# Kernel tuning notes

Measured on AMD Instinct MI355X. Metric: run time of the kernel, lower is better.

## Reference

```python
import jax, jax.numpy as jnp
import numpy as np

VOCAB = 9
D = 128      # EMBED_DIM
S = 64       # SEQ_LEN / context_length
B = 512      # batch
NH = 4       # num_heads
DH = D // NH # head dim = 32
NB = 2       # num_blocks
EPS = 1e-5


def setup_inputs() -> dict:
    key = jax.random.key(0)
    ks = jax.random.split(key, 10)
    rn = lambda k, shape: jax.random.normal(k, shape, jnp.float32) * 0.02
    return {
        "x": jax.random.randint(ks[0], (B, S), 0, VOCAB),
        "emb": rn(ks[1], (VOCAB, D)),
        "ln1_w": jnp.ones((NB, D), jnp.float32),          # pre-sLSTM LayerNorm weight
        "Wg": rn(ks[2], (NB, 4, NH, DH, DH)),             # headwise gate projections (i,f,z,o)
        "R": rn(ks[3], (NB, NH, DH, 4 * DH)),             # recurrent kernels per head
        "bias": rn(ks[4], (NB, NH, 4, DH)),               # cell bias per head/gate
        "gn_w": jnp.ones((NB, D), jnp.float32),           # multi-head (group) norm weight
        "ln2_w": jnp.ones((NB, D), jnp.float32),          # pre-FF LayerNorm weight
        "ff_up_w": rn(ks[5], (NB, 2 * D, D)),             # gated FF up projection
        "ff_down_w": rn(ks[6], (NB, D, D)),               # FF down projection
        "post_w": jnp.ones((D,), jnp.float32),            # post-blocks LayerNorm weight
        "proj_w": rn(ks[7], (VOCAB, D)),
        "proj_b": jnp.zeros((VOCAB,), jnp.float32),
    }


def _layernorm(x, w):
    mu = x.mean(-1, keepdims=True)
    var = x.var(-1, keepdims=True)
    return (x - mu) * jax.lax.rsqrt(var + EPS) * w


def _mh_groupnorm(h, w):
    # h: [B,S,NH,DH] -> normalize over DH per head, scale by per-channel w [D]
    mu = h.mean(-1, keepdims=True)
    var = h.var(-1, keepdims=True)
    hn = (h - mu) * jax.lax.rsqrt(var + EPS)
    return hn.reshape(h.shape[0], h.shape[1], D) * w


def _slstm_layer(xh, Wg, R, b):
    # xh: [B,S,NH,DH]; Wg: [4,NH,DH,DH]; R: [NH,DH,4*DH]; b: [NH,4,DH]
    gx = jnp.einsum('bsnh,gnkh->sbngk', xh, Wg)  # [S,B,NH,4,DH] gate preacts (i,f,z,o)

    def step(carry, g):
        h, c, n, m = carry  # each [B,NH,DH]
        ry = jnp.einsum('bnh,nhk->bnk', h, R).reshape(h.shape[0], NH, 4, DH)
        raw = g + ry + b
        i_r, f_r, z_r, o_r = raw[:, :, 0], raw[:, :, 1], raw[:, :, 2], raw[:, :, 3]
        logfplusm = m + jax.nn.log_sigmoid(f_r)
        mnew = jnp.maximum(i_r, logfplusm)            # stabilizer
        ig = jnp.exp(i_r - mnew)
        fg = jnp.exp(logfplusm - mnew)
        cnew = fg * c + ig * jnp.tanh(z_r)
        nnew = fg * n + ig
        hnew = jax.nn.sigmoid(o_r) * cnew / nnew
        return (hnew, cnew, nnew, mnew), hnew

    z0 = jnp.zeros((xh.shape[0], NH, DH), xh.dtype)
    _, hs = jax.lax.scan(step, (z0, z0, z0, z0), gx)
    return hs.transpose(1, 0, 2, 3)  # [B,S,NH,DH]


def reference(x, emb, ln1_w, Wg, R, bias, gn_w, ln2_w, ff_up_w, ff_down_w, post_w, proj_w, proj_b):
    h = emb[x]  # [B,S,D]
    for bi in range(NB):
        xn = _layernorm(h, ln1_w[bi])
        y = _slstm_layer(xn.reshape(h.shape[0], S, NH, DH), Wg[bi], R[bi], bias[bi])
        h = h + _mh_groupnorm(y, gn_w[bi])
        xn = _layernorm(h, ln2_w[bi])
        up = xn @ ff_up_w[bi].T                       # [B,S,2D]
        gate, upv = up[..., :D], up[..., D:]
        h = h + (jax.nn.gelu(gate, approximate=False) * upv) @ ff_down_w[bi].T
    h = _layernorm(h, post_w)
    return h @ proj_w.T + proj_b  # [B,S,VOCAB]
```

## Files before the change

kernel.cpp:

```cpp
#include <hip/hip_runtime.h>
#include <math.h>

#define D      128
#define S_LEN  64
#define B_SZ   512
#define NH     4
#define DH     32
#define NB     2
#define VOCAB  9
#define EPS    1e-5f
#define NTOK   (B_SZ * S_LEN)

template <int CTRL>
__device__ __forceinline__ float dppf(float x) {
    return __int_as_float(__builtin_amdgcn_update_dpp(
        0, __float_as_int(x), CTRL, 0xF, 0xF, true));
}
__device__ __forceinline__ float wsum64(float x) {
    x += dppf<0x111>(x);
    x += dppf<0x112>(x);
    x += dppf<0x114>(x);
    x += dppf<0x118>(x);
    x += dppf<0x142>(x);
    x += dppf<0x143>(x);
    return __int_as_float(__builtin_amdgcn_readlane(__float_as_int(x), 63));
}

__device__ __forceinline__ int xc3(int t, int c) { return c ^ (((t >> 1) & 7) << 2); }
__device__ __forceinline__ int xa (int t, int c) { return c ^ ((t & 7) << 2); }

__device__ __forceinline__ float dot4(float4 a, float4 b, float c) {
    c = fmaf(a.x, b.x, c);
    c = fmaf(a.y, b.y, c);
    c = fmaf(a.z, b.z, c);
    c = fmaf(a.w, b.w, c);
    return c;
}

__global__ __launch_bounds__(256) void k_embed(const int* __restrict__ x,
                                               const float* __restrict__ emb,
                                               float* __restrict__ h,
                                               float* __restrict__ stats)
{
    int lane = threadIdx.x & 63;
    int wv   = threadIdx.x >> 6;
    int tok  = blockIdx.x * 4 + wv;
    int xi   = x[tok];
    float2 v = ((const float2*)(emb + xi * D))[lane];
    ((float2*)(h + (size_t)tok * D))[lane] = v;
    float s1 = wsum64(v.x + v.y);
    float s2 = wsum64(v.x * v.x + v.y * v.y);
    float mu  = s1 * (1.0f / D);
    float var = s2 * (1.0f / D) - mu * mu;
    if (lane == 0) {
        stats[tok * 2]     = mu;
        stats[tok * 2 + 1] = rsqrtf(var + EPS);
    }
}

__global__ __launch_bounds__(64, 2) void k_gxscan(
    const float* __restrict__ Wg,
    const float* __restrict__ Rm,
    const float* __restrict__ bias,
    const float* __restrict__ lnw,
    const float* __restrict__ gnw,
    const float* __restrict__ stats,
    float* __restrict__ h)
{
    __shared__ float xl[64 * 32];

    int b    = blockIdx.x >> 2;
    int n    = blockIdx.x & 3;
    int lane = threadIdx.x;
    int e    = lane >> 1;
    int sub  = lane & 1;
    int colA = sub * DH + e;

    size_t tok0 = (size_t)b * S_LEN;

    {
        const float* hrow = h + (tok0 + lane) * D + n * DH;
        float2 st = ((const float2*)stats)[tok0 + lane];
        float mu = st.x, rs = st.y;
        #pragma unroll
        for (int q = 0; q < 8; ++q) {
            float4 v = *(const float4*)(hrow + q * 4);
            float4 o;
            o.x = (v.x - mu) * rs * lnw[n * DH + q * 4 + 0];
            o.y = (v.y - mu) * rs * lnw[n * DH + q * 4 + 1];
            o.z = (v.z - mu) * rs * lnw[n * DH + q * 4 + 2];
            o.w = (v.w - mu) * rs * lnw[n * DH + q * 4 + 3];
            *(float4*)&xl[lane * 32 + ((q ^ (lane & 7)) << 2)] = o;
        }
    }
    __syncthreads();

    int gA = sub;
    int gB = 2 + sub;
    const float* wrowA = Wg + ((size_t)(gA * NH + n) * DH + e) * DH;
    const float* wrowB = Wg + ((size_t)(gB * NH + n) * DH + e) * DH;
    float4 wgA[8], wgB[8], wrA[8], wrB[8];
    #pragma unroll
    for (int cc = 0; cc < 8; ++cc) {
        wgA[cc] = *(const float4*)(wrowA + cc * 4);
        wgB[cc] = *(const float4*)(wrowB + cc * 4);
        #pragma unroll
        for (int j = 0; j < 4; ++j) {
            ((float*)&wrA[cc])[j] = Rm[(n * DH + cc * 4 + j) * 128 + colA];
            ((float*)&wrB[cc])[j] = Rm[(n * DH + cc * 4 + j) * 128 + 64 + colA];
        }
    }
    float biasA = bias[(n * 4 + gA) * DH + e];
    float biasB = bias[(n * 4 + gB) * DH + e];
    float gw    = gnw[n * DH + e];

    auto gxpair = [&](int s, float& ga, float& gb) {
        float a0 = 0.f, a1 = 0.f, b0 = 0.f, b1 = 0.f;
        #pragma unroll
        for (int cc = 0; cc < 8; cc += 2) {
            float4 x0 = *(const float4*)&xl[s * 32 + ((cc ^ (s & 7)) << 2)];
            float4 x1 = *(const float4*)&xl[s * 32 + (((cc + 1) ^ (s & 7)) << 2)];
            a0 = dot4(x0, wgA[cc],     a0);
            a1 = dot4(x1, wgA[cc + 1], a1);
            b0 = dot4(x0, wgB[cc],     b0);
            b1 = dot4(x1, wgB[cc + 1], b1);
        }
        ga = biasA + (a0 + a1);
        gb = biasB + (b0 + b1);
    };

    float curA[8], curB[8], nxtA[8], nxtB[8];
    #pragma unroll
    for (int i = 0; i < 8; ++i) gxpair(i, curA[i], curB[i]);

    float hu[32];
    #pragma unroll
    for (int i = 0; i < 32; ++i) hu[i] = 0.f;
    float c = 0.f, nacc = 0.f, m = 0.f;

    float* hb = h + tok0 * D + n * DH;
    float pHR[4];
    #pragma unroll
    for (int k = 0; k < 4; ++k) pHR[k] = hb[k * D + e];

    for (int ch = 0; ch < 8; ++ch) {
        #pragma unroll
        for (int i = 0; i < 8; ++i) {
            int s = ch * 8 + i;
            if (ch < 7) gxpair(s + 8, nxtA[i], nxtB[i]);
            int sp = (s + 4 < S_LEN) ? s + 4 : S_LEN - 1;
            float nHR = hb[sp * D + e];

            float r0=0,r1=0,r2=0,r3=0,q0=0,q1=0,q2=0,q3=0;
            #pragma unroll
            for (int cc = 0; cc < 8; ++cc) {
                r0 = fmaf(hu[cc*4+0], wrA[cc].x, r0);
                r1 = fmaf(hu[cc*4+1], wrA[cc].y, r1);
                r2 = fmaf(hu[cc*4+2], wrA[cc].z, r2);
                r3 = fmaf(hu[cc*4+3], wrA[cc].w, r3);
                q0 = fmaf(hu[cc*4+0], wrB[cc].x, q0);
                q1 = fmaf(hu[cc*4+1], wrB[cc].y, q1);
                q2 = fmaf(hu[cc*4+2], wrB[cc].z, q2);
                q3 = fmaf(hu[cc*4+3], wrB[cc].w, q3);
            }
            float rawA = curA[i] + ((r0 + r1) + (r2 + r3));
            float rawB = curB[i] + ((q0 + q1) + (q2 + q3));

            float xA = dppf<0xB1>(rawA);
            float xB = dppf<0xB1>(rawB);
            float i_r = sub ? xA   : rawA;
            float f_r = sub ? rawA : xA;
            float z_r = sub ? xB   : rawB;
            float o_r = sub ? rawB : xB;

            float lsf  = fminf(f_r, 0.f)
                       - 0.69314718055994531f * __log2f(1.0f + __expf(-fabsf(f_r)));
            float lfm  = m + lsf;
            float mnew = fmaxf(i_r, lfm);
            float ig   = __expf(i_r - mnew);
            float fg   = __expf(lfm - mnew);
            float t    = __expf(2.f * z_r);
            float tz   = 1.f - 2.f / (t + 1.f);
            c    = fg * c + ig * tz;
            nacc = fg * nacc + ig;
            m    = mnew;
            float hv = c / (nacc * (1.f + __expf(-o_r)));

            float s1 = wsum64(hv);
            float s2 = wsum64(hv * hv);
            float mu2 = s1 * (1.f / 64.f);
            float var = s2 * (1.f / 64.f) - mu2 * mu2;
            float hn  = (hv - mu2) * rsqrtf(var + EPS) * gw;

            if (!sub) hb[s * D + e] = pHR[0] + hn;

            #pragma unroll
            for (int i2 = 0; i2 < 32; ++i2)
                hu[i2] = __int_as_float(
                    __builtin_amdgcn_readlane(__float_as_int(hv), 2 * i2));

            pHR[0]=pHR[1]; pHR[1]=pHR[2]; pHR[2]=pHR[3]; pHR[3]=nHR;
        }
        #pragma unroll
        for (int i = 0; i < 8; ++i) { curA[i] = nxtA[i]; curB[i] = nxtB[i]; }
    }
}

template <int LAST>
__global__ __launch_bounds__(256, 2) void k_ff(float* __restrict__ h,
                                               const float* __restrict__ ln2w,
                                               const float* __restrict__ wup,
                                               const float* __restrict__ wdn,
                                               float* __restrict__ stats_out,
                                               const float* __restrict__ lastw,
                                               const float* __restrict__ projw,
                                               const float* __restrict__ projb,
                                               float* __restrict__ out)
{
    __shared__ float xs[32 * 128];
    __shared__ float as_[32 * 64];
    __shared__ float wt[2 * 32 * 64];

    int tid  = threadIdx.x;
    int lane = tid & 63;
    int wv   = tid >> 6;
    size_t tok0 = (size_t)blockIdx.x * 32;

    for (int i = 0; i < 8; ++i) {
        int t = wv * 8 + i;
        const float* hp = h + (tok0 + t) * D;
        float v1 = hp[lane], v2 = hp[64 + lane];
        float s1 = wsum64(v1 + v2);
        float s2 = wsum64(v1 * v1 + v2 * v2);
        float mu = s1 * (1.0f / D);
        float rs = rsqrtf(s2 * (1.0f / D) - mu * mu + EPS);
        xs[t * D + xc3(t, lane)]      = (v1 - mu) * rs * ln2w[lane];
        xs[t * D + xc3(t, lane + 64)] = (v2 - mu) * rs * ln2w[64 + lane];
    }

    int q     = tid & 7;
    int r0    = tid >> 3;
    int goff0 = r0 * D + q * 4;
    int goff1 = (r0 + 32) * D + q * 4;
    int s0    = r0 ^ (q << 2);
    int kb    = q * 4;

    auto ffld = [&](int id, float4* pre) {
        int p = (id >= 6) ? 1 : 0;
        int j = id - p * 6;
        const float* b0;
        const float* b1;
        if (j < 4) { b0 = wup + (p * 64) * D + j * 32;
                     b1 = wup + (128 + p * 64) * D + j * 32; }
        else       { int jj = j - 4;
                     b0 = wdn + p * 64 + jj * 32;
                     b1 = wdn + 64 * D + p * 64 + jj * 32; }
        pre[0] = *(const float4*)(b0 + goff0);
        pre[1] = *(const float4*)(b0 + goff1);
        pre[2] = *(const float4*)(b1 + goff0);
        pre[3] = *(const float4*)(b1 + goff1);
    };
    auto fst = [&](const float4* pre) {
        #pragma unroll
        for (int cc = 0; cc < 4; ++cc) {
            const float* p0 = (const float*)&pre[0];
            const float* p1 = (const float*)&pre[1];
            const float* p2 = (const float*)&pre[2];
            const float* p3 = (const float*)&pre[3];
            wt[(kb + cc) * 64 + s0]           = p0[cc];
            wt[(kb + cc) * 64 + s0 + 32]      = p1[cc];
            wt[2048 + (kb + cc) * 64 + s0]      = p2[cc];
            wt[2048 + (kb + cc) * 64 + s0 + 32] = p3[cc];
        }
    };

    int ti = tid >> 4;
    int oi = tid & 15;
    int t0 = ti * 2;
    int o0 = oi * 4;

    float accd[2][2][4];
    #pragma unroll
    for (int a1 = 0; a1 < 2; ++a1)
        #pragma unroll
        for (int j = 0; j < 2; ++j)
            #pragma unroll
            for (int cc = 0; cc < 4; ++cc) accd[a1][j][cc] = 0.f;

    float4 pre[4];
    ffld(0, pre);
    int id = 1;

    #pragma unroll
    for (int p = 0; p < 2; ++p) {
        float accg[2][4], accv[2][4];
        #pragma unroll
        for (int j = 0; j < 2; ++j)
            #pragma unroll
            for (int cc = 0; cc < 4; ++cc) { accg[j][cc] = 0.f; accv[j][cc] = 0.f; }

        for (int c4 = 0; c4 < 4; ++c4) {
            __syncthreads();
            fst(pre);
            if (id < 12) ffld(id, pre);
            ++id;
            __syncthreads();
            int kc = c4 * 32;
            #pragma unroll
            for (int k4 = 0; k4 < 8; ++k4) {
                float4 a0 = *(const float4*)&xs[t0 * D + xc3(t0, kc + k4 * 4)];
                float4 a1v = *(const float4*)&xs[(t0 + 1) * D + xc3(t0 + 1, kc + k4 * 4)];
                int ws = k4 << 2;
                #pragma unroll
                for (int i = 0; i < 4; ++i) {
                    int k = k4 * 4 + i;
                    float4 bg = *(const float4*)&wt[k * 64 + (o0 ^ ws)];
                    float4 bv = *(const float4*)&wt[2048 + k * 64 + (o0 ^ ws)];
                    float ax0 = ((const float*)&a0)[i];
                    float ax1 = ((const float*)&a1v)[i];
                    accg[0][0] = fmaf(ax0, bg.x, accg[0][0]);
                    accg[0][1] = fmaf(ax0, bg.y, accg[0][1]);
                    accg[0][2] = fmaf(ax0, bg.z, accg[0][2]);
                    accg[0][3] = fmaf(ax0, bg.w, accg[0][3]);
                    accg[1][0] = fmaf(ax1, bg.x, accg[1][0]);
                    accg[1][1] = fmaf(ax1, bg.y, accg[1][1]);
                    accg[1][2] = fmaf(ax1, bg.z, accg[1][2]);
                    accg[1][3] = fmaf(ax1, bg.w, accg[1][3]);
                    accv[0][0] = fmaf(ax0, bv.x, accv[0][0]);
                    accv[0][1] = fmaf(ax0, bv.y, accv[0][1]);
                    accv[0][2] = fmaf(ax0, bv.z, accv[0][2]);
                    accv[0][3] = fmaf(ax0, bv.w, accv[0][3]);
                    accv[1][0] = fmaf(ax1, bv.x, accv[1][0]);
                    accv[1][1] = fmaf(ax1, bv.y, accv[1][1]);
                    accv[1][2] = fmaf(ax1, bv.z, accv[1][2]);
                    accv[1][3] = fmaf(ax1, bv.w, accv[1][3]);
                }
            }
        }
        #pragma unroll
        for (int j = 0; j < 2; ++j) {
            int t = t0 + j;
            float4 av;
            float* ap = (float*)&av;
            #pragma unroll
            for (int cc = 0; cc < 4; ++cc) {
                float g = accg[j][cc];
                float u = accv[j][cc];
                ap[cc] = 0.5f * g * (1.0f + erff(g * 0.70710678118654752f)) * u;
            }
            *(float4*)&as_[t * 64 + xa(t, o0)] = av;
        }
        for (int c2 = 0; c2 < 2; ++c2) {
            __syncthreads();
            fst(pre);
            if (id < 12) ffld(id, pre);
            ++id;
            __syncthreads();
            int kc = c2 * 32;
            #pragma unroll
            for (int k4 = 0; k4 < 8; ++k4) {
                float4 a0 = *(const float4*)&as_[t0 * 64 + xa(t0, kc + k4 * 4)];
                float4 a1v = *(const float4*)&as_[(t0 + 1) * 64 + xa(t0 + 1, kc + k4 * 4)];
                int ws = k4 << 2;
                #pragma unroll
                for (int i = 0; i < 4; ++i) {
                    int k = k4 * 4 + i;
                    float4 b0v = *(const float4*)&wt[k * 64 + (o0 ^ ws)];
                    float4 b1v = *(const float4*)&wt[2048 + k * 64 + (o0 ^ ws)];
                    float ax0 = ((const float*)&a0)[i];
                    float ax1 = ((const float*)&a1v)[i];
                    accd[0][0][0] = fmaf(ax0, b0v.x, accd[0][0][0]);
                    accd[0][0][1] = fmaf(ax0, b0v.y, accd[0][0][1]);
                    accd[0][0][2] = fmaf(ax0, b0v.z, accd[0][0][2]);
                    accd[0][0][3] = fmaf(ax0, b0v.w, accd[0][0][3]);
                    accd[0][1][0] = fmaf(ax1, b0v.x, accd[0][1][0]);
                    accd[0][1][1] = fmaf(ax1, b0v.y, accd[0][1][1]);
                    accd[0][1][2] = fmaf(ax1, b0v.z, accd[0][1][2]);
                    accd[0][1][3] = fmaf(ax1, b0v.w, accd[0][1][3]);
                    accd[1][0][0] = fmaf(ax0, b1v.x, accd[1][0][0]);
                    accd[1][0][1] = fmaf(ax0, b1v.y, accd[1][0][1]);
                    accd[1][0][2] = fmaf(ax0, b1v.z, accd[1][0][2]);
                    accd[1][0][3] = fmaf(ax0, b1v.w, accd[1][0][3]);
                    accd[1][1][0] = fmaf(ax1, b1v.x, accd[1][1][0]);
                    accd[1][1][1] = fmaf(ax1, b1v.y, accd[1][1][1]);
                    accd[1][1][2] = fmaf(ax1, b1v.z, accd[1][1][2]);
                    accd[1][1][3] = fmaf(ax1, b1v.w, accd[1][1][3]);
                }
            }
        }
    }

    #pragma unroll
    for (int j = 0; j < 2; ++j) {
        int t = t0 + j;
        size_t tok = tok0 + t;
        #pragma unroll
        for (int a1 = 0; a1 < 2; ++a1) {
            int cb = a1 * 64 + o0;
            float4 hres = *(const float4*)(h + tok * D + cb);
            float4 hn;
            hn.x = hres.x + accd[a1][j][0];
            hn.y = hres.y + accd[a1][j][1];
            hn.z = hres.z + accd[a1][j][2];
            hn.w = hres.w + accd[a1][j][3];
            if (!LAST) *(float4*)(h + tok * D + cb) = hn;
            *(float4*)&xs[t * D + xc3(t, cb)] = hn;
        }
    }
    __syncthreads();

    if (!LAST) {
        for (int i = 0; i < 8; ++i) {
            int t = wv * 8 + i;
            float v1 = xs[t * D + xc3(t, lane)];
            float v2 = xs[t * D + xc3(t, lane + 64)];
            float s1 = wsum64(v1 + v2);
            float s2 = wsum64(v1 * v1 + v2 * v2);
            float mu = s1 * (1.0f / D);
            float rs = rsqrtf(s2 * (1.0f / D) - mu * mu + EPS);
            if (lane == 0) {
                stats_out[(tok0 + t) * 2]     = mu;
                stats_out[(tok0 + t) * 2 + 1] = rs;
            }
        }
    } else {
        float pw1[VOCAB], pw2[VOCAB], pb[VOCAB];
        #pragma unroll
        for (int v = 0; v < VOCAB; ++v) {
            pw1[v] = projw[v * D + lane];
            pw2[v] = projw[v * D + 64 + lane];
            pb[v]  = projb[v];
        }
        for (int i = 0; i < 8; ++i) {
            int t = wv * 8 + i;
            float v1 = xs[t * D + xc3(t, lane)];
            float v2 = xs[t * D + xc3(t, lane + 64)];
            float s1 = wsum64(v1 + v2);
            float s2 = wsum64(v1 * v1 + v2 * v2);
            float mu = s1 * (1.0f / D);
            float rs = rsqrtf(s2 * (1.0f / D) - mu * mu + EPS);
            float x1 = (v1 - mu) * rs * lastw[lane];
            float x2 = (v2 - mu) * rs * lastw[64 + lane];
            #pragma unroll
            for (int v = 0; v < VOCAB; ++v) {
                float pp = wsum64(fmaf(x1, pw1[v], x2 * pw2[v]));
                if (lane == 0) out[(tok0 + t) * VOCAB + v] = pp + pb[v];
            }
        }
    }
}

extern "C" void kernel_launch(void* const* d_in, const int* in_sizes, int n_in,
                              void* d_out, int out_size, void* d_ws, size_t ws_size,
                              hipStream_t stream)
{
    const int*   x     = (const int*)  d_in[0];
    const float* emb   = (const float*)d_in[1];
    const float* ln1   = (const float*)d_in[2];
    const float* Wg    = (const float*)d_in[3];
    const float* Rm    = (const float*)d_in[4];
    const float* bias  = (const float*)d_in[5];
    const float* gnw   = (const float*)d_in[6];
    const float* ln2   = (const float*)d_in[7];
    const float* wup   = (const float*)d_in[8];
    const float* wdn   = (const float*)d_in[9];
    const float* postw = (const float*)d_in[10];
    const float* projw = (const float*)d_in[11];
    const float* projb = (const float*)d_in[12];
    float* out   = (float*)d_out;
    float* hbuf  = (float*)d_ws;
    float* stats = hbuf + (size_t)NTOK * D;

    k_embed<<<NTOK / 4, 256, 0, stream>>>(x, emb, hbuf, stats);

    for (int bi = 0; bi < NB; ++bi) {
        k_gxscan<<<B_SZ * NH, 64, 0, stream>>>(Wg + bi * 4 * NH * DH * DH,
                                               Rm + bi * NH * DH * 4 * DH,
                                               bias + bi * NH * 4 * DH,
                                               ln1 + bi * D,
                                               gnw + bi * D,
                                               stats, hbuf);
        if (bi == 0)
            k_ff<0><<<NTOK / 32, 256, 0, stream>>>(hbuf, ln2 + bi * D,
                                                   wup + bi * 2 * D * D,
                                                   wdn + bi * D * D,
                                                   stats, nullptr, nullptr,
                                                   nullptr, nullptr);
        else
            k_ff<1><<<NTOK / 32, 256, 0, stream>>>(hbuf, ln2 + bi * D,
                                                   wup + bi * 2 * D * D,
                                                   wdn + bi * D * D,
                                                   nullptr, postw, projw,
                                                   projb, out);
    }
}
```

Baseline: 354.7 us.

## Split gate-projection and recurrence into producer/consumer waves with shared-memory double buffer

The sLSTM scan kernel now runs two waves per block. One wave computes the input gate projections for the next chunk of 8 timesteps into a double-buffered shared array, while the other runs the serial recurrence on the current chunk. This takes the gate-projection FMAs and their weight registers off the latency-critical recurrent wave and should let it run at higher occupancy. The cost is a block barrier per chunk and a producer wave that sits idle for much of each chunk.

```diff
diff --git a/kernel.cpp b/kernel.cpp
--- a/kernel.cpp
+++ b/kernel.cpp
@@ -58,7 +58,7 @@
     }
 }
 
-__global__ __launch_bounds__(64, 2) void k_gxscan(
+__global__ __launch_bounds__(128, 4) void k_gxscan(
     const float* __restrict__ Wg,
     const float* __restrict__ Rm,
     const float* __restrict__ bias,
@@ -67,142 +67,170 @@
     const float* __restrict__ stats,
     float* __restrict__ h)
 {
-    __shared__ float xl[64 * 32];
+    __shared__ float xl[64][32];
+    __shared__ float gxb[2][8][128];
 
     int b    = blockIdx.x >> 2;
     int n    = blockIdx.x & 3;
-    int lane = threadIdx.x;
+    int tid  = threadIdx.x;
+    int wv   = tid >> 6;
+    int lane = tid & 63;
+    size_t tok0 = (size_t)b * S_LEN;
+
+    {
+        int t  = tid >> 1;
+        int hf = tid & 1;
+        const float* hrow = h + (tok0 + t) * D + n * DH + hf * 16;
+        float2 st = ((const float2*)stats)[tok0 + t];
+        float mu = st.x, rs = st.y;
+        #pragma unroll
+        for (int q = 0; q < 4; ++q) {
+            int qq = hf * 4 + q;
+            float4 v = *(const float4*)(hrow + q * 4);
+            float4 o;
+            o.x = (v.x - mu) * rs * lnw[n * DH + qq * 4 + 0];
+            o.y = (v.y - mu) * rs * lnw[n * DH + qq * 4 + 1];
+            o.z = (v.z - mu) * rs * lnw[n * DH + qq * 4 + 2];
+            o.w = (v.w - mu) * rs * lnw[n * DH + qq * 4 + 3];
+            *(float4*)&xl[t][(qq ^ (t & 7)) << 2] = o;
+        }
+    }
+
     int e    = lane >> 1;
     int sub  = lane & 1;
     int colA = sub * DH + e;
 
-    size_t tok0 = (size_t)b * S_LEN;
-
-    {
-        const float* hrow = h + (tok0 + lane) * D + n * DH;
-        float2 st = ((const float2*)stats)[tok0 + lane];
-        float mu = st.x, rs = st.y;
-        #pragma unroll
-        for (int q = 0; q < 8; ++q) {
-            float4 v = *(const float4*)(hrow + q * 4);
-            float4 o;
-            o.x = (v.x - mu) * rs * lnw[n * DH + q * 4 + 0];
-            o.y = (v.y - mu) * rs * lnw[n * DH + q * 4 + 1];
-            o.z = (v.z - mu) * rs * lnw[n * DH + q * 4 + 2];
-            o.w = (v.w - mu) * rs * lnw[n * DH + q * 4 + 3];
-            *(float4*)&xl[lane * 32 + ((q ^ (lane & 7)) << 2)] = o;
-        }
-    }
-    __syncthreads();
-
-    int gA = sub;
-    int gB = 2 + sub;
-    const float* wrowA = Wg + ((size_t)(gA * NH + n) * DH + e) * DH;
-    const float* wrowB = Wg + ((size_t)(gB * NH + n) * DH + e) * DH;
-    float4 wgA[8], wgB[8], wrA[8], wrB[8];
-    #pragma unroll
-    for (int cc = 0; cc < 8; ++cc) {
-        wgA[cc] = *(const float4*)(wrowA + cc * 4);
-        wgB[cc] = *(const float4*)(wrowB + cc * 4);
-        #pragma unroll
-        for (int j = 0; j < 4; ++j) {
-            ((float*)&wrA[cc])[j] = Rm[(n * DH + cc * 4 + j) * 128 + colA];
-            ((float*)&wrB[cc])[j] = Rm[(n * DH + cc * 4 + j) * 128 + 64 + colA];
-        }
-    }
-    float biasA = bias[(n * 4 + gA) * DH + e];
-    float biasB = bias[(n * 4 + gB) * DH + e];
-    float gw    = gnw[n * DH + e];
-
-    auto gxpair = [&](int s, float& ga, float& gb) {
-        float a0 = 0.f, a1 = 0.f, b0 = 0.f, b1 = 0.f;
-        #pragma unroll
-        for (int cc = 0; cc < 8; cc += 2) {
-            float4 x0 = *(const float4*)&xl[s * 32 + ((cc ^ (s & 7)) << 2)];
-            float4 x1 = *(const float4*)&xl[s * 32 + (((cc + 1) ^ (s & 7)) << 2)];
-            a0 = dot4(x0, wgA[cc],     a0);
-            a1 = dot4(x1, wgA[cc + 1], a1);
-            b0 = dot4(x0, wgB[cc],     b0);
-            b1 = dot4(x1, wgB[cc + 1], b1);
-        }
-        ga = biasA + (a0 + a1);
-        gb = biasB + (b0 + b1);
+    float4 wrA[8], wrB[8];
+    float4 wg1[8], wg2[8];
+    float  gw = 0.f, bs1 = 0.f, bs2 = 0.f;
+
+    if (wv == 0) {
+        #pragma unroll
+        for (int cc = 0; cc < 8; ++cc)
+            #pragma unroll
+            for (int j = 0; j < 4; ++j) {
+                ((float*)&wrA[cc])[j] = Rm[(n * DH + cc * 4 + j) * 128 + colA];
+                ((float*)&wrB[cc])[j] = Rm[(n * DH + cc * 4 + j) * 128 + 64 + colA];
+            }
+        gw = gnw[n * DH + e];
+    } else {
+        int g1 = lane >> 5, e1 = lane & 31;
+        int g2 = g1 + 2;
+        const float* r1 = Wg + ((size_t)(g1 * NH + n) * DH + e1) * DH;
+        const float* r2 = Wg + ((size_t)(g2 * NH + n) * DH + e1) * DH;
+        #pragma unroll
+        for (int cc = 0; cc < 8; ++cc) {
+            wg1[cc] = *(const float4*)(r1 + cc * 4);
+            wg2[cc] = *(const float4*)(r2 + cc * 4);
+        }
+        bs1 = bias[(n * 4 + g1) * DH + e1];
+        bs2 = bias[(n * 4 + g2) * DH + e1];
+    }
+
+    auto compute_chunk = [&](int ch) {
+        int bufi = ch & 1;
+        #pragma unroll
+        for (int i = 0; i < 8; ++i) {
+            int t = ch * 8 + i;
+            float a0 = 0.f, a1 = 0.f, b0 = 0.f, b1 = 0.f;
+            #pragma unroll
+            for (int cc = 0; cc < 8; cc += 2) {
+                float4 x0 = *(const float4*)&xl[t][(cc ^ (t & 7)) << 2];
+                float4 x1 = *(const float4*)&xl[t][((cc + 1) ^ (t & 7)) << 2];
+                a0 = dot4(x0, wg1[cc],     a0);
+                a1 = dot4(x1, wg1[cc + 1], a1);
+                b0 = dot4(x0, wg2[cc],     b0);
+                b1 = dot4(x1, wg2[cc + 1], b1);
+            }
+            gxb[bufi][i][lane]      = bs1 + (a0 + a1);
+            gxb[bufi][i][64 + lane] = bs2 + (b0 + b1);
+        }
     };
-
-    float curA[8], curB[8], nxtA[8], nxtB[8];
-    #pragma unroll
-    for (int i = 0; i < 8; ++i) gxpair(i, curA[i], curB[i]);
 
     float hu[32];
     #pragma unroll
     for (int i = 0; i < 32; ++i) hu[i] = 0.f;
     float c = 0.f, nacc = 0.f, m = 0.f;
-
     float* hb = h + tok0 * D + n * DH;
     float pHR[4];
-    #pragma unroll
-    for (int k = 0; k < 4; ++k) pHR[k] = hb[k * D + e];
+    if (wv == 0) {
+        #pragma unroll
+        for (int k = 0; k < 4; ++k) pHR[k] = hb[k * D + e];
+    }
+
+    __syncthreads();
+    if (wv == 1) compute_chunk(0);
+    __syncthreads();
 
     for (int ch = 0; ch < 8; ++ch) {
-        #pragma unroll
-        for (int i = 0; i < 8; ++i) {
-            int s = ch * 8 + i;
-            if (ch < 7) gxpair(s + 8, nxtA[i], nxtB[i]);
-            int sp = (s + 4 < S_LEN) ? s + 4 : S_LEN - 1;
-            float nHR = hb[sp * D + e];
-
-            float r0=0,r1=0,r2=0,r3=0,q0=0,q1=0,q2=0,q3=0;
-            #pragma unroll
-            for (int cc = 0; cc < 8; ++cc) {
-                r0 = fmaf(hu[cc*4+0], wrA[cc].x, r0);
-                r1 = fmaf(hu[cc*4+1], wrA[cc].y, r1);
-                r2 = fmaf(hu[cc*4+2], wrA[cc].z, r2);
-                r3 = fmaf(hu[cc*4+3], wrA[cc].w, r3);
-                q0 = fmaf(hu[cc*4+0], wrB[cc].x, q0);
-                q1 = fmaf(hu[cc*4+1], wrB[cc].y, q1);
-                q2 = fmaf(hu[cc*4+2], wrB[cc].z, q2);
-                q3 = fmaf(hu[cc*4+3], wrB[cc].w, q3);
-            }
-            float rawA = curA[i] + ((r0 + r1) + (r2 + r3));
-            float rawB = curB[i] + ((q0 + q1) + (q2 + q3));
-
-            float xA = dppf<0xB1>(rawA);
-            float xB = dppf<0xB1>(rawB);
-            float i_r = sub ? xA   : rawA;
-            float f_r = sub ? rawA : xA;
-            float z_r = sub ? xB   : rawB;
-            float o_r = sub ? rawB : xB;
-
-            float lsf  = fminf(f_r, 0.f)
-                       - 0.69314718055994531f * __log2f(1.0f + __expf(-fabsf(f_r)));
-            float lfm  = m + lsf;
-            float mnew = fmaxf(i_r, lfm);
-            float ig   = __expf(i_r - mnew);
-            float fg   = __expf(lfm - mnew);
-            float t    = __expf(2.f * z_r);
-            float tz   = 1.f - 2.f / (t + 1.f);
-            c    = fg * c + ig * tz;
-            nacc = fg * nacc + ig;
-            m    = mnew;
-            float hv = c / (nacc * (1.f + __expf(-o_r)));
-
-            float s1 = wsum64(hv);
-            float s2 = wsum64(hv * hv);
-            float mu2 = s1 * (1.f / 64.f);
-            float var = s2 * (1.f / 64.f) - mu2 * mu2;
-            float hn  = (hv - mu2) * rsqrtf(var + EPS) * gw;
-
-            if (!sub) hb[s * D + e] = pHR[0] + hn;
-
-            #pragma unroll
-            for (int i2 = 0; i2 < 32; ++i2)
-                hu[i2] = __int_as_float(
-                    __builtin_amdgcn_readlane(__float_as_int(hv), 2 * i2));
-
-            pHR[0]=pHR[1]; pHR[1]=pHR[2]; pHR[2]=pHR[3]; pHR[3]=nHR;
-        }
-        #pragma unroll
-        for (int i = 0; i < 8; ++i) { curA[i] = nxtA[i]; curB[i] = nxtB[i]; }
+        if (wv == 1) {
+            if (ch < 7) compute_chunk(ch + 1);
+        } else {
+            int bufi = ch & 1;
+            float gA_[8], gB_[8];
+            #pragma unroll
+            for (int i = 0; i < 8; ++i) {
+                gA_[i] = gxb[bufi][i][colA];
+                gB_[i] = gxb[bufi][i][64 + colA];
+            }
+            #pragma unroll
+            for (int i = 0; i < 8; ++i) {
+                int s = ch * 8 + i;
+                int sp = (s + 4 < S_LEN) ? s + 4 : S_LEN - 1;
+                float nHR = hb[sp * D + e];
+
+                float r0=0,r1=0,r2=0,r3=0,q0=0,q1=0,q2=0,q3=0;
+                #pragma unroll
+                for (int cc = 0; cc < 8; ++cc) {
+                    r0 = fmaf(hu[cc*4+0], wrA[cc].x, r0);
+                    r1 = fmaf(hu[cc*4+1], wrA[cc].y, r1);
+                    r2 = fmaf(hu[cc*4+2], wrA[cc].z, r2);
+                    r3 = fmaf(hu[cc*4+3], wrA[cc].w, r3);
+                    q0 = fmaf(hu[cc*4+0], wrB[cc].x, q0);
+                    q1 = fmaf(hu[cc*4+1], wrB[cc].y, q1);
+                    q2 = fmaf(hu[cc*4+2], wrB[cc].z, q2);
+                    q3 = fmaf(hu[cc*4+3], wrB[cc].w, q3);
+                }
+                float rawA = gA_[i] + ((r0 + r1) + (r2 + r3));
+                float rawB = gB_[i] + ((q0 + q1) + (q2 + q3));
+
+                float xA = dppf<0xB1>(rawA);
+                float xB = dppf<0xB1>(rawB);
+                float i_r = sub ? xA   : rawA;
+                float f_r = sub ? rawA : xA;
+                float z_r = sub ? xB   : rawB;
+                float o_r = sub ? rawB : xB;
+
+                float lsf  = fminf(f_r, 0.f)
+                           - 0.69314718055994531f * __log2f(1.0f + __expf(-fabsf(f_r)));
+                float lfm  = m + lsf;
+                float mnew = fmaxf(i_r, lfm);
+                float ig   = __expf(i_r - mnew);
+                float fg   = __expf(lfm - mnew);
+                float t    = __expf(2.f * z_r);
+                float tz   = 1.f - 2.f / (t + 1.f);
+                c    = fg * c + ig * tz;
+                nacc = fg * nacc + ig;
+                m    = mnew;
+                float hv = c / (nacc * (1.f + __expf(-o_r)));
+
+                float s1 = wsum64(hv);
+                float s2 = wsum64(hv * hv);
+                float mu2 = s1 * (1.f / 64.f);
+                float var = s2 * (1.f / 64.f) - mu2 * mu2;
+                float hn  = (hv - mu2) * rsqrtf(var + EPS) * gw;
+
+                if (!sub) hb[s * D + e] = pHR[0] + hn;
+
+                #pragma unroll
+                for (int i2 = 0; i2 < 32; ++i2)
+                    hu[i2] = __int_as_float(
+                        __builtin_amdgcn_readlane(__float_as_int(hv), 2 * i2));
+
+                pHR[0]=pHR[1]; pHR[1]=pHR[2]; pHR[2]=pHR[3]; pHR[3]=nHR;
+            }
+        }
+        __syncthreads();
     }
 }
 
@@ -474,12 +502,12 @@
     k_embed<<<NTOK / 4, 256, 0, stream>>>(x, emb, hbuf, stats);
 
     for (int bi = 0; bi < NB; ++bi) {
-        k_gxscan<<<B_SZ * NH, 64, 0, stream>>>(Wg + bi * 4 * NH * DH * DH,
-                                               Rm + bi * NH * DH * 4 * DH,
-                                               bias + bi * NH * 4 * DH,
-                                               ln1 + bi * D,
-                                               gnw + bi * D,
-                                               stats, hbuf);
+        k_gxscan<<<B_SZ * NH, 128, 0, stream>>>(Wg + bi * 4 * NH * DH * DH,
+                                                Rm + bi * NH * DH * 4 * DH,
+                                                bias + bi * NH * 4 * DH,
+                                                ln1 + bi * D,
+                                                gnw + bi * D,
+                                                stats, hbuf);
         if (bi == 0)
             k_ff<0><<<NTOK / 32, 256, 0, stream>>>(hbuf, ln2 + bi * D,
                                                    wup + bi * 2 * D * D,
```

Measured after the change: 1.413 ms. +298.5%, slower.
